# Performance work log

Hardware: AMD Instinct MI355X
Metric: run time of the kernel (lower is better)

Reference implementation:

```python
import jax, jax.numpy as jnp
import numpy as np

EPS = 1e-5
DEPTH = 3
NQ = 12


def _bn(x, g, b):
    # BatchNorm1d in training mode: batch statistics, biased variance
    mu = x.mean(0)
    var = x.var(0)
    return (x - mu) / jnp.sqrt(var + EPS) * g + b


def _ln(x, g, b):
    mu = x.mean(-1, keepdims=True)
    var = x.var(-1, keepdims=True)
    return (x - mu) / jnp.sqrt(var + EPS) * g + b


def _apply_1q(s, U, q):
    # s: [B, 2^NQ] complex; U: [2,2] (shared) or [B,2,2] (per-sample); qubit q = q-th MSB
    B = s.shape[0]
    s = s.reshape(B, 2 ** q, 2, -1)
    sub = 'ij,bajc->baic' if U.ndim == 2 else 'bij,bajc->baic'
    return jnp.einsum(sub, U, s).reshape(B, -1)


def _apply_cry(s, theta, c):
    # controlled-Ry(theta): control qubit c, target qubit c+1 (adjacent)
    B = s.shape[0]
    s = s.reshape(B, 2 ** c, 2, 2, -1)
    co = jnp.cos(theta / 2).astype(s.dtype)
    si = jnp.sin(theta / 2).astype(s.dtype)
    s1 = s[:, :, 1]  # control = |1> block
    new1 = jnp.stack([co * s1[:, :, 0] - si * s1[:, :, 1],
                      si * s1[:, :, 0] + co * s1[:, :, 1]], axis=2)
    s = jnp.concatenate([s[:, :, :1], new1[:, :, None]], axis=2)
    return s.reshape(B, -1)


def _measure(s):
    # P(qubit q measures |1>) for each qubit
    p = jnp.abs(s) ** 2  # [B, 2^NQ]
    B = p.shape[0]
    probs = [p.reshape(B, 2 ** q, 2, -1).sum(axis=(1, 3))[:, 1] for q in range(NQ)]
    return jnp.stack(probs, axis=1)  # [B, NQ]


def _rot_mats(rot):
    # fused Rz(rz) @ Ry(ry) @ Rx(rx) for each (depth, qubit) -> [DEPTH, NQ, 2, 2]
    hx, hy, hz = rot[..., 0] / 2, rot[..., 1] / 2, rot[..., 2] / 2
    cx, sx = jnp.cos(hx), jnp.sin(hx)
    Rx = jnp.stack([jnp.stack([cx + 0j, -1j * sx], -1),
                    jnp.stack([-1j * sx, cx + 0j], -1)], -2)
    cy, sy = jnp.cos(hy), jnp.sin(hy)
    Ry = jnp.stack([jnp.stack([cy, -sy], -1),
                    jnp.stack([sy, cy], -1)], -2).astype(jnp.complex64)
    ez = jnp.exp(-1j * hz)
    z0 = jnp.zeros_like(ez)
    Rz = jnp.stack([jnp.stack([ez, z0], -1),
                    jnp.stack([z0, jnp.conj(ez)], -1)], -2)
    return jnp.einsum('...ij,...jk,...kl->...il', Rz, Ry, Rx).astype(jnp.complex64)


def _quantum_layer(x, We, be, gi, bi, rot, ent, Wd, bd, go, bo):
    e = jnp.tanh(_bn(x @ We.T + be, gi, bi))  # [B, NQ]
    nrm = jnp.linalg.norm(e, axis=1, keepdims=True)
    a = jnp.where(nrm > 0, e / nrm, e)        # per-sample L2-normalized amplitudes
    B = x.shape[0]
    s = jnp.zeros((B, 2 ** NQ), jnp.complex64).at[:, 0].set(1.0)
    # amplitude encoding: Ry(2*arcsin(|a|)) then phase pi (sign) if a<0 -> diag(1,-1)@Ry
    ang = 2.0 * jnp.arcsin(jnp.clip(jnp.abs(a), 0.0, 1.0))
    c, si = jnp.cos(ang / 2), jnp.sin(ang / 2)
    sg = jnp.where(a < 0, -1.0, 1.0)
    for q in range(NQ):
        U = jnp.stack([jnp.stack([c[:, q], -si[:, q]], -1),
                       jnp.stack([sg[:, q] * si[:, q], sg[:, q] * c[:, q]], -1)],
                      -2).astype(jnp.complex64)  # [B,2,2]
        s = _apply_1q(s, U, q)
    # parameterized circuit: per-qubit fused Rz.Ry.Rx, then nearest-neighbor CRy chain
    U = _rot_mats(rot)
    for d in range(DEPTH):
        for q in range(NQ):
            s = _apply_1q(s, U[d, q], q)
        for i in range(NQ - 1):
            s = _apply_cry(s, ent[d, i], i)
    m = _measure(s)
    return _bn(m @ Wd.T + bd, go, bo)


def setup_inputs() -> dict:
    key = jax.random.key(0)
    ks = jax.random.split(key, 16)
    B, IN, H1, H2, H3, OUT = 512, 512, 512, 512, 1024, 256

    def lin(k, o, i):
        k1, k2 = jax.random.split(k)
        lim = 1.0 / np.sqrt(i)
        return (jax.random.uniform(k1, (o, i), jnp.float32, -lim, lim),
                jax.random.uniform(k2, (o,), jnp.float32, -lim, lim))

    qWe0, qbe0 = lin(ks[1], NQ, IN)
    qWd0, qbd0 = lin(ks[2], H1, NQ)
    qWe1, qbe1 = lin(ks[3], NQ, H1)
    qWd1, qbd1 = lin(ks[4], H2, NQ)
    W2, b2 = lin(ks[5], H3, H2)
    Wo, bo = lin(ks[6], OUT, H3)
    return {
        'x': jax.random.normal(ks[0], (B, IN), jnp.float32),
        'qWe0': qWe0, 'qbe0': qbe0,
        'qgi0': jnp.ones(NQ), 'qbi0': jnp.zeros(NQ),
        'rot0': 0.1 * jax.random.normal(ks[7], (DEPTH, NQ, 3), jnp.float32),
        'ent0': 0.1 * jax.random.normal(ks[8], (DEPTH, NQ - 1), jnp.float32),
        'qWd0': qWd0, 'qbd0': qbd0,
        'qgo0': jnp.ones(H1), 'qbo0': jnp.zeros(H1),
        'qWe1': qWe1, 'qbe1': qbe1,
        'qgi1': jnp.ones(NQ), 'qbi1': jnp.zeros(NQ),
        'rot1': 0.1 * jax.random.normal(ks[9], (DEPTH, NQ, 3), jnp.float32),
        'ent1': 0.1 * jax.random.normal(ks[10], (DEPTH, NQ - 1), jnp.float32),
        'qWd1': qWd1, 'qbd1': qbd1,
        'qgo1': jnp.ones(H2), 'qbo1': jnp.zeros(H2),
        'W2': W2, 'b2': b2, 'ln2g': jnp.ones(H3), 'ln2b': jnp.zeros(H3),
        'Wo': Wo, 'bo': bo, 'lnog': jnp.ones(OUT), 'lnob': jnp.zeros(OUT),
    }


def reference(x, qWe0, qbe0, qgi0, qbi0, rot0, ent0, qWd0, qbd0, qgo0, qbo0,
              qWe1, qbe1, qgi1, qbi1, rot1, ent1, qWd1, qbd1, qgo1, qbo1,
              W2, b2, ln2g, ln2b, Wo, bo, lnog, lnob):
    h = _quantum_layer(x, qWe0, qbe0, qgi0, qbi0, rot0, ent0, qWd0, qbd0, qgo0, qbo0)
    h = _quantum_layer(h, qWe1, qbe1, qgi1, qbi1, rot1, ent1, qWd1, qbd1, qgo1, qbo1)
    h = jax.nn.relu(_ln(h @ W2.T + b2, ln2g, ln2b))  # classical block (dropout = identity, eval)
    return _ln(h @ Wo.T + bo, lnog, lnob)
```

## Files before the change

### kernel.cpp

```cpp
#include <hip/hip_runtime.h>
#include <math.h>

#define EPS   1e-5f
#define NQ    12
#define DEPTH 3
#define BATCH 512
#define DIM   4096

__device__ inline float2 cmul(float2 a, float2 b) {
    return make_float2(a.x*b.x - a.y*b.y, a.x*b.y + a.y*b.x);
}
__device__ inline float2 cmac2(float2 ua, float2 s, float2 ub, float2 p) {
    return make_float2(ua.x*s.x - ua.y*s.y + ub.x*p.x - ub.y*p.y,
                       ua.x*s.y + ua.y*s.x + ub.x*p.y + ub.y*p.x);
}
__device__ inline float fast_tanh(float x) {
    float e = __expf(2.f * x);
    return 1.f - 2.f * __builtin_amdgcn_rcpf(e + 1.f);
}

__device__ inline int swz(int a) { return a ^ ((a >> 4) & 15); }

template<int HB> __device__ inline int ampl16(int t, int k) {
    return ((t >> HB) << (HB+4)) | (k << HB) | (t & ((1<<HB)-1));
}

__device__ inline void remap16a(float2* amp, float2* lds,
                                const int* wA, const int* rA) {
    #pragma unroll
    for (int k = 0; k < 16; ++k) lds[wA[k]] = amp[k];
    __syncthreads();
    #pragma unroll
    for (int k = 0; k < 16; ++k) amp[k] = lds[rA[k]];
}

template<int BP>
__device__ inline void one_q(float2* amp, float2 u00, float2 u01, float2 u10, float2 u11) {
    #pragma unroll
    for (int g = 0; g < 8; ++g) {
        const int j0 = ((g >> BP) << (BP+1)) | (g & ((1<<BP)-1));
        const int j1 = j0 | (1 << BP);
        float2 a0 = amp[j0], a1 = amp[j1];
        amp[j0] = cmac2(u00, a0, u01, a1);
        amp[j1] = cmac2(u10, a0, u11, a1);
    }
}

template<int CB, int TB>
__device__ inline void cry_rr(float2* amp, float co, float si) {
    #pragma unroll
    for (int m = 0; m < 16; ++m) {
        if (((m >> CB) & 1) && !((m >> TB) & 1)) {
            const int j1 = m | (1 << TB);
            float2 a0 = amp[m], a1 = amp[j1];
            amp[m]  = make_float2(co*a0.x - si*a1.x, co*a0.y - si*a1.y);
            amp[j1] = make_float2(si*a0.x + co*a1.x, si*a0.y + co*a1.y);
        }
    }
}

template<int TB>
__device__ inline void crysel16(float2* amp, int ctrl, float co, float si) {
    float co2 = ctrl ? co : 1.f;
    float s2  = ctrl ? si : 0.f;
    #pragma unroll
    for (int m = 0; m < 16; ++m) {
        if (!((m >> TB) & 1)) {
            const int j1 = m | (1 << TB);
            float2 a0 = amp[m], a1 = amp[j1];
            amp[m]  = make_float2(co2*a0.x - s2*a1.x, co2*a0.y - s2*a1.y);
            amp[j1] = make_float2(s2*a0.x + co2*a1.x, s2*a0.y + co2*a1.y);
        }
    }
}

__device__ void consts_body(int t,
        const float* rot0, const float* ent0, const float* rot1, const float* ent1,
        float2* Uc, float2* Cc) {
    if (t < 72) {
        int layer = t / 36, rem = t % 36, d = rem / 12, q = rem % 12;
        const float* rot = layer ? rot1 : rot0;
        float hx = 0.5f * rot[(d*NQ + q)*3 + 0];
        float hy = 0.5f * rot[(d*NQ + q)*3 + 1];
        float hz = 0.5f * rot[(d*NQ + q)*3 + 2];
        float cx = cosf(hx), sx = sinf(hx);
        float cy = cosf(hy), sy = sinf(hy);
        float2 m00 = make_float2( cy*cx,  sy*sx);
        float2 m01 = make_float2(-sy*cx, -cy*sx);
        float2 m10 = make_float2( sy*cx, -cy*sx);
        float2 m11 = make_float2( cy*cx, -sy*sx);
        float2 ez  = make_float2(cosf(hz), -sinf(hz));
        float2 ezc = make_float2(ez.x, -ez.y);
        float2* U = Uc + t*4;
        U[0] = cmul(ez,  m00);
        U[1] = cmul(ez,  m01);
        U[2] = cmul(ezc, m10);
        U[3] = cmul(ezc, m11);
    } else if (t < 72 + 66) {
        int idx = t - 72, layer = idx / 33, rem = idx % 33;
        const float* ent = layer ? ent1 : ent0;
        float th = 0.5f * ent[rem];
        Cc[idx] = make_float2(cosf(th), sinf(th));
    }
}

__global__ __launch_bounds__(256) void encode0_consts_kernel(
        const float* __restrict__ X, const float* __restrict__ We,
        const float* __restrict__ be, float* __restrict__ Yraw,
        const float* __restrict__ rot0, const float* __restrict__ ent0,
        const float* __restrict__ rot1, const float* __restrict__ ent1,
        float2* __restrict__ Uc, float2* __restrict__ Cc,
        float* __restrict__ Yraw1z) {
    int tid = threadIdx.x;
    if (blockIdx.x == 128) {
        consts_body(tid, rot0, ent0, rot1, ent1, Uc, Cc);
        for (int i = tid; i < BATCH*NQ; i += 256) Yraw1z[i] = 0.f;
        return;
    }
    __shared__ float w[NQ][512];
    {
        const float4* src = (const float4*)We;
        float4* dst = (float4*)&w[0][0];
        #pragma unroll
        for (int i = tid; i < NQ*128; i += 256) dst[i] = src[i];
    }
    __syncthreads();
    int wave = tid >> 6, lane = tid & 63;
    int b = blockIdx.x * 4 + wave;
    const float4* xr = (const float4*)(X + (size_t)b * 512);
    float acc[NQ] = {};
    #pragma unroll
    for (int j = 0; j < 2; ++j) {
        float4 xv = xr[lane + 64*j];
        #pragma unroll
        for (int q = 0; q < NQ; ++q) {
            float4 wv = ((const float4*)&w[q][0])[lane + 64*j];
            acc[q] += xv.x*wv.x + xv.y*wv.y + xv.z*wv.z + xv.w*wv.w;
        }
    }
    #pragma unroll
    for (int q = 0; q < NQ; ++q) {
        float v = acc[q];
        #pragma unroll
        for (int off = 32; off; off >>= 1) v += __shfl_xor(v, off);
        if (lane == q) Yraw[b*NQ + q] = v + be[q];
    }
}

__global__ __launch_bounds__(256, 2) void qsim3w_kernel(
        const float* __restrict__ Yraw, const float* __restrict__ gi,
        const float* __restrict__ bi, const float2* __restrict__ UcAll,
        const float2* __restrict__ CcAll, int layer,
        float* __restrict__ mout) {
    int blk = blockIdx.x, t = threadIdx.x;
    const float2* Uc = UcAll + layer * DEPTH * NQ * 4;
    const float2* Cc = CcAll + layer * DEPTH * (NQ - 1);
    __shared__ float2 lds2[2][DIM];
    __shared__ float sred[96];

    int A8[16], A4[16], A0[16];
    #pragma unroll
    for (int k = 0; k < 16; ++k) {
        A8[k] = swz(ampl16<8>(t, k));
        A4[k] = swz(ampl16<4>(t, k));
        A0[k] = swz(ampl16<0>(t, k));
    }

    float sum[NQ] = {}, sq[NQ] = {};
    {
        const float4* Y4 = (const float4*)Yraw;
        #pragma unroll
        for (int j = 0; j < 6; ++j) {
            float4 v = Y4[t*6 + j];
            int q0 = (j*4) % 12;
            sum[q0+0]+=v.x; sq[q0+0]+=v.x*v.x;
            sum[q0+1]+=v.y; sq[q0+1]+=v.y*v.y;
            sum[q0+2]+=v.z; sq[q0+2]+=v.z*v.z;
            sum[q0+3]+=v.w; sq[q0+3]+=v.w*v.w;
        }
    }
    int lane = t & 63, wave = t >> 6;
    #pragma unroll
    for (int q = 0; q < NQ; ++q) {
        #pragma unroll
        for (int off = 32; off; off >>= 1) {
            sum[q] += __shfl_xor(sum[q], off);
            sq[q]  += __shfl_xor(sq[q],  off);
        }
    }
    if (lane == 0) {
        #pragma unroll
        for (int q = 0; q < NQ; ++q) {
            sred[wave*24 + q]      = sum[q];
            sred[wave*24 + 12 + q] = sq[q];
        }
    }
    __syncthreads();
    float a[NQ]; float n2 = 0.f;
    const float* yr = Yraw + blk*NQ;
    #pragma unroll
    for (int q = 0; q < NQ; ++q) {
        float s  = sred[q]    + sred[24+q] + sred[48+q] + sred[72+q];
        float s2 = sred[12+q] + sred[36+q] + sred[60+q] + sred[84+q];
        float mu  = s  * (1.f/512.f);
        float var = s2 * (1.f/512.f) - mu*mu;
        float val = (yr[q] - mu) * rsqrtf(var + EPS) * gi[q] + bi[q];
        a[q] = fast_tanh(val);
        n2 += a[q]*a[q];
    }
    float scn = (n2 > 0.f) ? rsqrtf(n2) : 1.f;
    #pragma unroll
    for (int q = 0; q < NQ; ++q) a[q] *= scn;

    float2 v0[NQ], v1[NQ];
    #pragma unroll
    for (int q = 0; q < NQ; ++q) {
        float sv = fminf(fabsf(a[q]), 1.f);
        float c  = sqrtf(fmaxf(1.f - sv*sv, 0.f));
        float ss = (a[q] < 0.f) ? -sv : sv;
        const float2* U = Uc + q*4;
        v0[q] = make_float2(U[0].x*c + U[1].x*ss, U[0].y*c + U[1].y*ss);
        v1[q] = make_float2(U[2].x*c + U[3].x*ss, U[2].y*c + U[3].y*ss);
    }
    float2 common = make_float2(1.f, 0.f);
    #pragma unroll
    for (int j = 0; j < 8; ++j)
        common = cmul(common, ((t >> j) & 1) ? v1[11-j] : v0[11-j]);
    float2 amp[16];
    amp[0] = common;
    #pragma unroll
    for (int mb = 0; mb < 4; ++mb) {
        const int qb = 3 - mb;
        #pragma unroll
        for (int k = 0; k < (1<<mb); ++k) {
            amp[k | (1<<mb)] = cmul(amp[k], v1[qb]);
            amp[k]           = cmul(amp[k], v0[qb]);
        }
    }

    int rb = 0;
    for (int d = 0; d < DEPTH; ++d) {
        const float2* Ud = Uc + d*NQ*4;
        const float2* Cd = Cc + d*(NQ-1);
        if (d > 0) {
            remap16a(amp, lds2[rb], A0, A8); rb ^= 1;
            one_q<3>(amp, Ud[0],  Ud[1],  Ud[2],  Ud[3]);
            one_q<2>(amp, Ud[4],  Ud[5],  Ud[6],  Ud[7]);
            one_q<1>(amp, Ud[8],  Ud[9],  Ud[10], Ud[11]);
            one_q<0>(amp, Ud[12], Ud[13], Ud[14], Ud[15]);
        }
        cry_rr<3,2>(amp, Cd[0].x, Cd[0].y);
        cry_rr<2,1>(amp, Cd[1].x, Cd[1].y);
        cry_rr<1,0>(amp, Cd[2].x, Cd[2].y);
        remap16a(amp, lds2[rb], A8, A4); rb ^= 1;
        if (d > 0) {
            one_q<3>(amp, Ud[16], Ud[17], Ud[18], Ud[19]);
            one_q<2>(amp, Ud[20], Ud[21], Ud[22], Ud[23]);
            one_q<1>(amp, Ud[24], Ud[25], Ud[26], Ud[27]);
            one_q<0>(amp, Ud[28], Ud[29], Ud[30], Ud[31]);
        }
        crysel16<3>(amp, (t >> 4) & 1, Cd[3].x, Cd[3].y);
        cry_rr<3,2>(amp, Cd[4].x, Cd[4].y);
        cry_rr<2,1>(amp, Cd[5].x, Cd[5].y);
        cry_rr<1,0>(amp, Cd[6].x, Cd[6].y);
        remap16a(amp, lds2[rb], A4, A0); rb ^= 1;
        if (d > 0) {
            one_q<3>(amp, Ud[32], Ud[33], Ud[34], Ud[35]);
            one_q<2>(amp, Ud[36], Ud[37], Ud[38], Ud[39]);
            one_q<1>(amp, Ud[40], Ud[41], Ud[42], Ud[43]);
            one_q<0>(amp, Ud[44], Ud[45], Ud[46], Ud[47]);
        }
        crysel16<3>(amp, t & 1, Cd[7].x, Cd[7].y);
        cry_rr<3,2>(amp, Cd[8].x,  Cd[8].y);
        cry_rr<2,1>(amp, Cd[9].x,  Cd[9].y);
        cry_rr<1,0>(amp, Cd[10].x, Cd[10].y);
    }

    float msum = 0.f, p8 = 0.f, p9 = 0.f, p10 = 0.f, p11 = 0.f;
    #pragma unroll
    for (int k = 0; k < 16; ++k) {
        float m = amp[k].x*amp[k].x + amp[k].y*amp[k].y;
        msum += m;
        if (k & 8) p8  += m;
        if (k & 4) p9  += m;
        if (k & 2) p10 += m;
        if (k & 1) p11 += m;
    }
    #pragma unroll
    for (int q = 0; q < NQ; ++q) {
        float v;
        if (q < 8)        v = ((t >> (7-q)) & 1) ? msum : 0.f;
        else if (q == 8)  v = p8;
        else if (q == 9)  v = p9;
        else if (q == 10) v = p10;
        else              v = p11;
        #pragma unroll
        for (int off = 32; off; off >>= 1) v += __shfl_xor(v, off);
        if (lane == 0) sred[q*4 + wave] = v;
    }
    __syncthreads();
    if (t < NQ)
        mout[blk*16 + t] = sred[t*4] + sred[t*4+1] + sred[t*4+2] + sred[t*4+3];
}

__global__ __launch_bounds__(512) void decode_kernel(
        const float* __restrict__ m, const float* __restrict__ Wd,
        const float* __restrict__ bd, const float* __restrict__ go,
        const float* __restrict__ bo, float* __restrict__ outT) {
    int h = blockIdx.x, b = threadIdx.x;
    __shared__ float2 red[8];
    float4 r0 = *(const float4*)(m + (size_t)b*16 + 0);
    float4 r1 = *(const float4*)(m + (size_t)b*16 + 4);
    float4 r2 = *(const float4*)(m + (size_t)b*16 + 8);
    const float4* W4 = (const float4*)(Wd + h*NQ);
    float4 w0 = W4[0], w1 = W4[1], w2 = W4[2];
    float z = bd[h]
        + r0.x*w0.x + r0.y*w0.y + r0.z*w0.z + r0.w*w0.w
        + r1.x*w1.x + r1.y*w1.y + r1.z*w1.z + r1.w*w1.w
        + r2.x*w2.x + r2.y*w2.y + r2.z*w2.z + r2.w*w2.w;
    float2 v = make_float2(z, z*z);
    int lane = b & 63, wave = b >> 6;
    for (int off = 32; off; off >>= 1) { v.x += __shfl_down(v.x, off); v.y += __shfl_down(v.y, off); }
    if (lane == 0) red[wave] = v;
    __syncthreads();
    float s = 0.f, s2 = 0.f;
    #pragma unroll
    for (int wv = 0; wv < 8; ++wv) { s += red[wv].x; s2 += red[wv].y; }
    float mu  = s  * (1.f/512.f);
    float var = s2 * (1.f/512.f) - mu*mu;
    outT[(size_t)h*BATCH + b] = (z - mu) * rsqrtf(var + EPS) * go[h] + bo[h];
}

__global__ __launch_bounds__(256) void encode1_kernel(
        const float* __restrict__ h1T, const float* __restrict__ We,
        const float* __restrict__ be, float* __restrict__ Yraw1) {
    __shared__ float w[NQ][512];
    __shared__ float red[4*64*NQ];
    int tid = threadIdx.x, blk = blockIdx.x;
    {
        const float4* src = (const float4*)We;
        float4* dst = (float4*)&w[0][0];
        #pragma unroll
        for (int i = tid; i < NQ*128; i += 256) dst[i] = src[i];
    }
    __syncthreads();
    int kc = blk >> 3, bc = blk & 7;
    int bl = tid & 63, hg = tid >> 6;
    int b = bc*64 + bl;
    float acc[NQ] = {};
    #pragma unroll
    for (int i = 0; i < 16; ++i) {
        int h = kc*64 + hg*16 + i;
        float xv = h1T[(size_t)h*512 + b];
        #pragma unroll
        for (int q = 0; q < NQ; ++q) acc[q] += xv * w[q][h];
    }
    #pragma unroll
    for (int q = 0; q < NQ; ++q) red[(hg*64 + bl)*NQ + q] = acc[q];
    __syncthreads();
    for (int i = tid; i < 64*NQ; i += 256) {
        int bl2 = i / NQ, q = i - bl2*NQ;
        float v = red[bl2*NQ+q] + red[(64+bl2)*NQ+q] + red[(128+bl2)*NQ+q] + red[(192+bl2)*NQ+q];
        if (kc == 0) v += be[q];
        atomicAdd(&Yraw1[(size_t)(bc*64 + bl2)*NQ + q], v);
    }
}

__global__ __launch_bounds__(256) void gemm1_kernel(
        const float* __restrict__ AT, const float* __restrict__ W,
        float* __restrict__ Cpart) {
    __shared__ float As[2][32][64];
    __shared__ float Bs[2][32][68];
    const int b0 = blockIdx.x * 64, j0 = blockIdx.y * 64;
    const int kbase = blockIdx.z * 128;
    float* C = Cpart + (size_t)blockIdx.z * 512 * 1024;
    const int tid = threadIdx.x;
    const int tr = tid >> 4, tc = tid & 15;
    const int a_kk = tid >> 4, a_f4 = tid & 15;
    const int b_jj = tid >> 3, b_k4 = (tid & 7) * 4;
    float4 ra0, ra1, rb0, rb1;
    float acc[4][4] = {};
    {
        const int k0 = kbase;
        ra0 = *(const float4*)(AT + (size_t)(k0 + a_kk)*512 + b0 + a_f4*4);
        ra1 = *(const float4*)(AT + (size_t)(k0 + a_kk + 16)*512 + b0 + a_f4*4);
        rb0 = *(const float4*)(W + (size_t)(j0 + b_jj)*512 + k0 + b_k4);
        rb1 = *(const float4*)(W + (size_t)(j0 + b_jj + 32)*512 + k0 + b_k4);
        *(float4*)&As[0][a_kk][a_f4*4] = ra0;
        *(float4*)&As[0][a_kk+16][a_f4*4] = ra1;
        Bs[0][b_k4+0][b_jj] = rb0.x; Bs[0][b_k4+1][b_jj] = rb0.y;
        Bs[0][b_k4+2][b_jj] = rb0.z; Bs[0][b_k4+3][b_jj] = rb0.w;
        Bs[0][b_k4+0][b_jj+32] = rb1.x; Bs[0][b_k4+1][b_jj+32] = rb1.y;
        Bs[0][b_k4+2][b_jj+32] = rb1.z; Bs[0][b_k4+3][b_jj+32] = rb1.w;
    }
    __syncthreads();
    for (int s = 0; s < 4; ++s) {
        if (s < 3) {
            const int k0 = kbase + (s+1)*32;
            ra0 = *(const float4*)(AT + (size_t)(k0 + a_kk)*512 + b0 + a_f4*4);
            ra1 = *(const float4*)(AT + (size_t)(k0 + a_kk + 16)*512 + b0 + a_f4*4);
            rb0 = *(const float4*)(W + (size_t)(j0 + b_jj)*512 + k0 + b_k4);
            rb1 = *(const float4*)(W + (size_t)(j0 + b_jj + 32)*512 + k0 + b_k4);
        }
        const int bf = s & 1;
        #pragma unroll
        for (int kk = 0; kk < 32; ++kk) {
            float4 a  = *(const float4*)&As[bf][kk][tr*4];
            float4 bv = *(const float4*)&Bs[bf][kk][tc*4];
            acc[0][0] += a.x*bv.x; acc[0][1] += a.x*bv.y; acc[0][2] += a.x*bv.z; acc[0][3] += a.x*bv.w;
            acc[1][0] += a.y*bv.x; acc[1][1] += a.y*bv.y; acc[1][2] += a.y*bv.z; acc[1][3] += a.y*bv.w;
            acc[2][0] += a.z*bv.x; acc[2][1] += a.z*bv.y; acc[2][2] += a.z*bv.z; acc[2][3] += a.z*bv.w;
            acc[3][0] += a.w*bv.x; acc[3][1] += a.w*bv.y; acc[3][2] += a.w*bv.z; acc[3][3] += a.w*bv.w;
        }
        if (s < 3) {
            const int nb = bf ^ 1;
            *(float4*)&As[nb][a_kk][a_f4*4] = ra0;
            *(float4*)&As[nb][a_kk+16][a_f4*4] = ra1;
            Bs[nb][b_k4+0][b_jj] = rb0.x; Bs[nb][b_k4+1][b_jj] = rb0.y;
            Bs[nb][b_k4+2][b_jj] = rb0.z; Bs[nb][b_k4+3][b_jj] = rb0.w;
            Bs[nb][b_k4+0][b_jj+32] = rb1.x; Bs[nb][b_k4+1][b_jj+32] = rb1.y;
            Bs[nb][b_k4+2][b_jj+32] = rb1.z; Bs[nb][b_k4+3][b_jj+32] = rb1.w;
        }
        __syncthreads();
    }
    #pragma unroll
    for (int r = 0; r < 4; ++r) {
        float4 o = make_float4(acc[r][0], acc[r][1], acc[r][2], acc[r][3]);
        *(float4*)(C + (size_t)(b0 + tr*4 + r)*1024 + j0 + tc*4) = o;
    }
}

__global__ __launch_bounds__(256) void ln_relu_kernel(
        const float* __restrict__ P, const float* __restrict__ bias,
        const float* __restrict__ g, const float* __restrict__ be,
        float* __restrict__ Y) {
    int b = blockIdx.x, tid = threadIdx.x;
    __shared__ float2 red[4];
    float v[4];
    #pragma unroll
    for (int j = 0; j < 4; ++j) {
        int col = tid + j*256;
        float t = bias[col];
        #pragma unroll
        for (int z = 0; z < 4; ++z) t += P[(size_t)z*524288 + (size_t)b*1024 + col];
        v[j] = t;
    }
    float2 r = make_float2(v[0]+v[1]+v[2]+v[3],
                           v[0]*v[0]+v[1]*v[1]+v[2]*v[2]+v[3]*v[3]);
    int lane = tid & 63, wave = tid >> 6;
    for (int off = 32; off; off >>= 1) { r.x += __shfl_down(r.x, off); r.y += __shfl_down(r.y, off); }
    if (lane == 0) red[wave] = r;
    __syncthreads();
    float s = red[0].x + red[1].x + red[2].x + red[3].x;
    float s2 = red[0].y + red[1].y + red[2].y + red[3].y;
    float mu  = s  * (1.f/1024.f);
    float var = s2 * (1.f/1024.f) - mu*mu;
    float inv = rsqrtf(var + EPS);
    float* yr = Y + (size_t)b * 1024;
    #pragma unroll
    for (int j = 0; j < 4; ++j) {
        int col = tid + j*256;
        yr[col] = fmaxf((v[j]-mu)*inv*g[col] + be[col], 0.f);
    }
}

__global__ __launch_bounds__(256) void gemm2_kernel(
        const float* __restrict__ Amat, const float* __restrict__ W,
        float* __restrict__ Cpart) {
    __shared__ __align__(16) char smem[27000];
    float (*As)[32][36] = (float(*)[32][36])smem;
    float (*Bs)[32][68] = (float(*)[32][68])(smem + 9216);
    const int b0 = blockIdx.x * 32, j0 = blockIdx.y * 64;
    const int kbase = blockIdx.z * 128;
    float* C = Cpart + (size_t)blockIdx.z * 512 * 256;
    const int tid = threadIdx.x;
    const int tr = tid >> 4, tc = tid & 15;
    const int l_r = tid >> 3, l_k4 = (tid & 7) * 4;
    float4 ra0, rb0, rb1;
    float acc[2][4] = {};
    {
        const int k0 = kbase;
        ra0 = *(const float4*)(Amat + (size_t)(b0 + l_r)*1024 + k0 + l_k4);
        rb0 = *(const float4*)(W + (size_t)(j0 + l_r)*1024 + k0 + l_k4);
        rb1 = *(const float4*)(W + (size_t)(j0 + l_r + 32)*1024 + k0 + l_k4);
        As[0][l_k4+0][l_r] = ra0.x; As[0][l_k4+1][l_r] = ra0.y;
        As[0][l_k4+2][l_r] = ra0.z; As[0][l_k4+3][l_r] = ra0.w;
        Bs[0][l_k4+0][l_r] = rb0.x; Bs[0][l_k4+1][l_r] = rb0.y;
        Bs[0][l_k4+2][l_r] = rb0.z; Bs[0][l_k4+3][l_r] = rb0.w;
        Bs[0][l_k4+0][l_r+32] = rb1.x; Bs[0][l_k4+1][l_r+32] = rb1.y;
        Bs[0][l_k4+2][l_r+32] = rb1.z; Bs[0][l_k4+3][l_r+32] = rb1.w;
    }
    __syncthreads();
    for (int s = 0; s < 4; ++s) {
        if (s < 3) {
            const int k0 = kbase + (s+1)*32;
            ra0 = *(const float4*)(Amat + (size_t)(b0 + l_r)*1024 + k0 + l_k4);
            rb0 = *(const float4*)(W + (size_t)(j0 + l_r)*1024 + k0 + l_k4);
            rb1 = *(const float4*)(W + (size_t)(j0 + l_r + 32)*1024 + k0 + l_k4);
        }
        const int bf = s & 1;
        #pragma unroll
        for (int kk = 0; kk < 32; ++kk) {
            float a0 = As[bf][kk][tr*2], a1 = As[bf][kk][tr*2+1];
            float4 bv = *(const float4*)&Bs[bf][kk][tc*4];
            acc[0][0] += a0*bv.x; acc[0][1] += a0*bv.y; acc[0][2] += a0*bv.z; acc[0][3] += a0*bv.w;
            acc[1][0] += a1*bv.x; acc[1][1] += a1*bv.y; acc[1][2] += a1*bv.z; acc[1][3] += a1*bv.w;
        }
        if (s < 3) {
            const int nb = bf ^ 1;
            As[nb][l_k4+0][l_r] = ra0.x; As[nb][l_k4+1][l_r] = ra0.y;
            As[nb][l_k4+2][l_r] = ra0.z; As[nb][l_k4+3][l_r] = ra0.w;
            Bs[nb][l_k4+0][l_r] = rb0.x; Bs[nb][l_k4+1][l_r] = rb0.y;
            Bs[nb][l_k4+2][l_r] = rb0.z; Bs[nb][l_k4+3][l_r] = rb0.w;
            Bs[nb][l_k4+0][l_r+32] = rb1.x; Bs[nb][l_k4+1][l_r+32] = rb1.y;
            Bs[nb][l_k4+2][l_r+32] = rb1.z; Bs[nb][l_k4+3][l_r+32] = rb1.w;
        }
        __syncthreads();
    }
    #pragma unroll
    for (int r = 0; r < 2; ++r) {
        float4 o = make_float4(acc[r][0], acc[r][1], acc[r][2], acc[r][3]);
        *(float4*)(C + (size_t)(b0 + tr*2 + r)*256 + j0 + tc*4) = o;
    }
}

__global__ __launch_bounds__(256) void ln_out_kernel(
        const float* __restrict__ P, const float* __restrict__ bias,
        const float* __restrict__ g, const float* __restrict__ be,
        float* __restrict__ Y) {
    int b = blockIdx.x, tid = threadIdx.x;
    __shared__ float2 red[4];
    float v0 = bias[tid];
    #pragma unroll
    for (int z = 0; z < 8; ++z) v0 += P[(size_t)z*131072 + (size_t)b*256 + tid];
    float2 v = make_float2(v0, v0*v0);
    int lane = tid & 63, wave = tid >> 6;
    for (int off = 32; off; off >>= 1) { v.x += __shfl_down(v.x, off); v.y += __shfl_down(v.y, off); }
    if (lane == 0) red[wave] = v;
    __syncthreads();
    float s = red[0].x + red[1].x + red[2].x + red[3].x;
    float s2 = red[0].y + red[1].y + red[2].y + red[3].y;
    float mu  = s  * (1.f/256.f);
    float var = s2 * (1.f/256.f) - mu*mu;
    Y[(size_t)b*256 + tid] = (v0 - mu) * rsqrtf(var + EPS) * g[tid] + be[tid];
}

extern "C" void kernel_launch(void* const* d_in, const int* in_sizes, int n_in,
                              void* d_out, int out_size, void* d_ws, size_t ws_size,
                              hipStream_t stream) {
    const float* x    = (const float*)d_in[0];
    const float* qWe0 = (const float*)d_in[1];
    const float* qbe0 = (const float*)d_in[2];
    const float* qgi0 = (const float*)d_in[3];
    const float* qbi0 = (const float*)d_in[4];
    const float* rot0 = (const float*)d_in[5];
    const float* ent0 = (const float*)d_in[6];
    const float* qWd0 = (const float*)d_in[7];
    const float* qbd0 = (const float*)d_in[8];
    const float* qgo0 = (const float*)d_in[9];
    const float* qbo0 = (const float*)d_in[10];
    const float* qWe1 = (const float*)d_in[11];
    const float* qbe1 = (const float*)d_in[12];
    const float* qgi1 = (const float*)d_in[13];
    const float* qbi1 = (const float*)d_in[14];
    const float* rot1 = (const float*)d_in[15];
    const float* ent1 = (const float*)d_in[16];
    const float* qWd1 = (const float*)d_in[17];
    const float* qbd1 = (const float*)d_in[18];
    const float* qgo1 = (const float*)d_in[19];
    const float* qbo1 = (const float*)d_in[20];
    const float* W2   = (const float*)d_in[21];
    const float* b2   = (const float*)d_in[22];
    const float* ln2g = (const float*)d_in[23];
    const float* ln2b = (const float*)d_in[24];
    const float* Wo   = (const float*)d_in[25];
    const float* bo   = (const float*)d_in[26];
    const float* lnog = (const float*)d_in[27];
    const float* lnob = (const float*)d_in[28];
    float* out = (float*)d_out;
    float* ws  = (float*)d_ws;

    float2* Uc   = (float2*)ws;
    float2* Cc   = Uc + 288;
    float* Yraw0 = ws + 1024;
    float* m0    = ws + 8192;
    float* Yraw1 = ws + 16384;
    float* m1    = ws + 24576;
    float* h1T   = ws + 65536;
    float* h2T   = ws + 589824;
    float* t3p   = ws + 851968;
    float* t3n   = ws + 2949120;
    float* t4p   = ws + 3473408;

    hipLaunchKernelGGL(encode0_consts_kernel, dim3(129), dim3(256), 0, stream,
                       x, qWe0, qbe0, Yraw0, rot0, ent0, rot1, ent1, Uc, Cc, Yraw1);
    hipLaunchKernelGGL(qsim3w_kernel, dim3(512), dim3(256), 0, stream,
                       Yraw0, qgi0, qbi0, Uc, Cc, 0, m0);
    hipLaunchKernelGGL(decode_kernel, dim3(512), dim3(512), 0, stream,
                       m0, qWd0, qbd0, qgo0, qbo0, h1T);
    hipLaunchKernelGGL(encode1_kernel, dim3(64), dim3(256), 0, stream,
                       h1T, qWe1, qbe1, Yraw1);
    hipLaunchKernelGGL(qsim3w_kernel, dim3(512), dim3(256), 0, stream,
                       Yraw1, qgi1, qbi1, Uc, Cc, 1, m1);
    hipLaunchKernelGGL(decode_kernel, dim3(512), dim3(512), 0, stream,
                       m1, qWd1, qbd1, qgo1, qbo1, h2T);
    hipLaunchKernelGGL(gemm1_kernel, dim3(8, 16, 4), dim3(256), 0, stream,
                       h2T, W2, t3p);
    hipLaunchKernelGGL(ln_relu_kernel, dim3(512), dim3(256), 0, stream,
                       t3p, b2, ln2g, ln2b, t3n);
    hipLaunchKernelGGL(gemm2_kernel, dim3(16, 4, 8), dim3(256), 0, stream,
                       t3n, Wo, t4p);
    hipLaunchKernelGGL(ln_out_kernel, dim3(512), dim3(256), 0, stream,
                       t4p, bo, lnog, lnob, out);
}
```

Measured before the change: 220.2 us.

## Fuse decode0 and encode1 algebraically into a single-block mid kernel

Replaces the layer-0 decode (512x512 BatchNorm output) and the layer-1 encode GEMM with one single-block kernel. It uses the fact that decode is affine in the 12-dim measurement vector, so batch stats follow from the mean and covariance of m0, and the encode can be folded into a 12x12 matrix plus a bias. The second qsim then reads precomputed normalised angles instead of recomputing BatchNorm and tanh, and the Yraw1 zeroing and atomics go away. In exchange, all of this runs on one workgroup with serial loops, and the covariance-based variance may change floating-point rounding.

New measurement: 229.4 us. +4.2%, slower.

```diff
diff --git a/kernel.cpp b/kernel.cpp
--- a/kernel.cpp
+++ b/kernel.cpp
@@ -109,12 +109,10 @@
         const float* __restrict__ be, float* __restrict__ Yraw,
         const float* __restrict__ rot0, const float* __restrict__ ent0,
         const float* __restrict__ rot1, const float* __restrict__ ent1,
-        float2* __restrict__ Uc, float2* __restrict__ Cc,
-        float* __restrict__ Yraw1z) {
+        float2* __restrict__ Uc, float2* __restrict__ Cc) {
     int tid = threadIdx.x;
     if (blockIdx.x == 128) {
         consts_body(tid, rot0, ent0, rot1, ent1, Uc, Cc);
-        for (int i = tid; i < BATCH*NQ; i += 256) Yraw1z[i] = 0.f;
         return;
     }
     __shared__ float w[NQ][512];
@@ -147,8 +145,9 @@
     }
 }
 
+template<int MODE>
 __global__ __launch_bounds__(256, 2) void qsim3w_kernel(
-        const float* __restrict__ Yraw, const float* __restrict__ gi,
+        const float* __restrict__ Yin, const float* __restrict__ gi,
         const float* __restrict__ bi, const float2* __restrict__ UcAll,
         const float2* __restrict__ CcAll, int layer,
         float* __restrict__ mout) {
@@ -166,51 +165,59 @@
         A0[k] = swz(ampl16<0>(t, k));
     }
 
-    float sum[NQ] = {}, sq[NQ] = {};
-    {
-        const float4* Y4 = (const float4*)Yraw;
-        #pragma unroll
-        for (int j = 0; j < 6; ++j) {
-            float4 v = Y4[t*6 + j];
-            int q0 = (j*4) % 12;
-            sum[q0+0]+=v.x; sq[q0+0]+=v.x*v.x;
-            sum[q0+1]+=v.y; sq[q0+1]+=v.y*v.y;
-            sum[q0+2]+=v.z; sq[q0+2]+=v.z*v.z;
-            sum[q0+3]+=v.w; sq[q0+3]+=v.w*v.w;
-        }
-    }
-    int lane = t & 63, wave = t >> 6;
-    #pragma unroll
-    for (int q = 0; q < NQ; ++q) {
-        #pragma unroll
-        for (int off = 32; off; off >>= 1) {
-            sum[q] += __shfl_xor(sum[q], off);
-            sq[q]  += __shfl_xor(sq[q],  off);
-        }
-    }
-    if (lane == 0) {
+    float a[NQ];
+    if (MODE == 0) {
+        float sum[NQ] = {}, sq[NQ] = {};
+        {
+            const float4* Y4 = (const float4*)Yin;
+            #pragma unroll
+            for (int j = 0; j < 6; ++j) {
+                float4 v = Y4[t*6 + j];
+                int q0 = (j*4) % 12;
+                sum[q0+0]+=v.x; sq[q0+0]+=v.x*v.x;
+                sum[q0+1]+=v.y; sq[q0+1]+=v.y*v.y;
+                sum[q0+2]+=v.z; sq[q0+2]+=v.z*v.z;
+                sum[q0+3]+=v.w; sq[q0+3]+=v.w*v.w;
+            }
+        }
+        int lane = t & 63, wave = t >> 6;
         #pragma unroll
         for (int q = 0; q < NQ; ++q) {
-            sred[wave*24 + q]      = sum[q];
-            sred[wave*24 + 12 + q] = sq[q];
-        }
-    }
-    __syncthreads();
-    float a[NQ]; float n2 = 0.f;
-    const float* yr = Yraw + blk*NQ;
-    #pragma unroll
-    for (int q = 0; q < NQ; ++q) {
-        float s  = sred[q]    + sred[24+q] + sred[48+q] + sred[72+q];
-        float s2 = sred[12+q] + sred[36+q] + sred[60+q] + sred[84+q];
-        float mu  = s  * (1.f/512.f);
-        float var = s2 * (1.f/512.f) - mu*mu;
-        float val = (yr[q] - mu) * rsqrtf(var + EPS) * gi[q] + bi[q];
-        a[q] = fast_tanh(val);
-        n2 += a[q]*a[q];
-    }
-    float scn = (n2 > 0.f) ? rsqrtf(n2) : 1.f;
-    #pragma unroll
-    for (int q = 0; q < NQ; ++q) a[q] *= scn;
+            #pragma unroll
+            for (int off = 32; off; off >>= 1) {
+                sum[q] += __shfl_xor(sum[q], off);
+                sq[q]  += __shfl_xor(sq[q],  off);
+            }
+        }
+        if (lane == 0) {
+            #pragma unroll
+            for (int q = 0; q < NQ; ++q) {
+                sred[wave*24 + q]      = sum[q];
+                sred[wave*24 + 12 + q] = sq[q];
+            }
+        }
+        __syncthreads();
+        float n2 = 0.f;
+        const float* yr = Yin + blk*NQ;
+        #pragma unroll
+        for (int q = 0; q < NQ; ++q) {
+            float s  = sred[q]    + sred[24+q] + sred[48+q] + sred[72+q];
+            float s2 = sred[12+q] + sred[36+q] + sred[60+q] + sred[84+q];
+            float mu  = s  * (1.f/512.f);
+            float var = s2 * (1.f/512.f) - mu*mu;
+            float val = (yr[q] - mu) * rsqrtf(var + EPS) * gi[q] + bi[q];
+            a[q] = fast_tanh(val);
+            n2 += a[q]*a[q];
+        }
+        float scn = (n2 > 0.f) ? rsqrtf(n2) : 1.f;
+        #pragma unroll
+        for (int q = 0; q < NQ; ++q) a[q] *= scn;
+        __syncthreads();
+    } else {
+        const float* ar = Yin + blk*16;
+        #pragma unroll
+        for (int q = 0; q < NQ; ++q) a[q] = ar[q];
+    }
 
     float2 v0[NQ], v1[NQ];
     #pragma unroll
@@ -286,6 +293,7 @@
         if (k & 2) p10 += m;
         if (k & 1) p11 += m;
     }
+    int lane = t & 63, wave = t >> 6;
     #pragma unroll
     for (int q = 0; q < NQ; ++q) {
         float v;
@@ -301,6 +309,127 @@
     __syncthreads();
     if (t < NQ)
         mout[blk*16 + t] = sred[t*4] + sred[t*4+1] + sred[t*4+2] + sred[t*4+3];
+}
+
+__global__ __launch_bounds__(512) void fuse_mid_kernel(
+        const float* __restrict__ m0,
+        const float* __restrict__ Wd, const float* __restrict__ bd,
+        const float* __restrict__ go, const float* __restrict__ bo,
+        const float* __restrict__ We1, const float* __restrict__ be1,
+        const float* __restrict__ gi1, const float* __restrict__ bi1,
+        float* __restrict__ A1) {
+    const int t = threadIdx.x;
+    __shared__ float mc[512][12];
+    __shared__ float su[512];
+    __shared__ float part[312][4];
+    __shared__ float mbar_s[12], C_s[144], E_s[144], F_s[12], mY[12], vY[12];
+
+    float mr[12];
+    {
+        float4 r0 = *(const float4*)(m0 + (size_t)t*16 + 0);
+        float4 r1 = *(const float4*)(m0 + (size_t)t*16 + 4);
+        float4 r2 = *(const float4*)(m0 + (size_t)t*16 + 8);
+        mr[0]=r0.x; mr[1]=r0.y; mr[2]=r0.z; mr[3]=r0.w;
+        mr[4]=r1.x; mr[5]=r1.y; mr[6]=r1.z; mr[7]=r1.w;
+        mr[8]=r2.x; mr[9]=r2.y; mr[10]=r2.z; mr[11]=r2.w;
+        #pragma unroll
+        for (int j = 0; j < 12; ++j) mc[t][j] = mr[j];
+    }
+    __syncthreads();
+    if (t < 48) {
+        int j = t >> 2, c = t & 3;
+        float s = 0.f;
+        for (int b = c*128; b < c*128 + 128; ++b) s += mc[b][j];
+        part[j][c] = s;
+    }
+    __syncthreads();
+    if (t < 12) mbar_s[t] = (part[t][0]+part[t][1]+part[t][2]+part[t][3]) * (1.f/512.f);
+    __syncthreads();
+    if (t < 312) {
+        int p = t >> 2, c = t & 3;
+        int j = 0, rem = p;
+        while (rem >= 12 - j) { rem -= 12 - j; ++j; }
+        int k = j + rem;
+        float s = 0.f;
+        for (int b = c*128; b < c*128 + 128; ++b) s += mc[b][j]*mc[b][k];
+        part[p][c] = s;
+    }
+    __syncthreads();
+    if (t < 78) {
+        int p = t, j = 0, rem = p;
+        while (rem >= 12 - j) { rem -= 12 - j; ++j; }
+        int k = j + rem;
+        float cv = (part[p][0]+part[p][1]+part[p][2]+part[p][3]) * (1.f/512.f)
+                   - mbar_s[j]*mbar_s[k];
+        C_s[j*12+k] = cv; C_s[k*12+j] = cv;
+    }
+    __syncthreads();
+    {
+        float wd[12];
+        #pragma unroll
+        for (int j = 0; j < 12; ++j) wd[j] = Wd[t*12 + j];
+        float mu = bd[t];
+        #pragma unroll
+        for (int j = 0; j < 12; ++j) mu += wd[j]*mbar_s[j];
+        float var = 0.f;
+        #pragma unroll
+        for (int j = 0; j < 12; ++j) {
+            float cj = 0.f;
+            #pragma unroll
+            for (int k = 0; k < 12; ++k) cj += C_s[j*12+k]*wd[k];
+            var += wd[j]*cj;
+        }
+        float s = go[t] * rsqrtf(var + EPS);
+        su[t] = bo[t] + s*(bd[t] - mu);
+        #pragma unroll
+        for (int j = 0; j < 12; ++j) mc[t][j] = s*wd[j];
+    }
+    __syncthreads();
+    if (t < 144) {
+        int q = t / 12, j = t - (t/12)*12;
+        const float* we = We1 + q*512;
+        float s = 0.f;
+        for (int h = 0; h < 512; ++h) s += we[h]*mc[h][j];
+        E_s[t] = s;
+    } else if (t < 156) {
+        int q = t - 144;
+        const float* we = We1 + q*512;
+        float s = be1[q];
+        for (int h = 0; h < 512; ++h) s += we[h]*su[h];
+        F_s[q] = s;
+    }
+    __syncthreads();
+    if (t < 12) {
+        float me = F_s[t];
+        #pragma unroll
+        for (int j = 0; j < 12; ++j) me += E_s[t*12+j]*mbar_s[j];
+        mY[t] = me;
+        float var = 0.f;
+        #pragma unroll
+        for (int j = 0; j < 12; ++j) {
+            float cj = 0.f;
+            #pragma unroll
+            for (int k = 0; k < 12; ++k) cj += C_s[j*12+k]*E_s[t*12+k];
+            var += E_s[t*12+j]*cj;
+        }
+        vY[t] = var;
+    }
+    __syncthreads();
+    {
+        float a[12]; float n2 = 0.f;
+        #pragma unroll
+        for (int q = 0; q < 12; ++q) {
+            float y = F_s[q];
+            #pragma unroll
+            for (int j = 0; j < 12; ++j) y += mr[j]*E_s[q*12+j];
+            float val = (y - mY[q]) * rsqrtf(vY[q] + EPS) * gi1[q] + bi1[q];
+            a[q] = fast_tanh(val);
+            n2 += a[q]*a[q];
+        }
+        float scn = (n2 > 0.f) ? rsqrtf(n2) : 1.f;
+        #pragma unroll
+        for (int q = 0; q < 12; ++q) A1[(size_t)t*16 + q] = a[q]*scn;
+    }
 }
 
 __global__ __launch_bounds__(512) void decode_kernel(
@@ -329,41 +458,6 @@
     float mu  = s  * (1.f/512.f);
     float var = s2 * (1.f/512.f) - mu*mu;
     outT[(size_t)h*BATCH + b] = (z - mu) * rsqrtf(var + EPS) * go[h] + bo[h];
-}
-
-__global__ __launch_bounds__(256) void encode1_kernel(
-        const float* __restrict__ h1T, const float* __restrict__ We,
-        const float* __restrict__ be, float* __restrict__ Yraw1) {
-    __shared__ float w[NQ][512];
-    __shared__ float red[4*64*NQ];
-    int tid = threadIdx.x, blk = blockIdx.x;
-    {
-        const float4* src = (const float4*)We;
-        float4* dst = (float4*)&w[0][0];
-        #pragma unroll
-        for (int i = tid; i < NQ*128; i += 256) dst[i] = src[i];
-    }
-    __syncthreads();
-    int kc = blk >> 3, bc = blk & 7;
-    int bl = tid & 63, hg = tid >> 6;
-    int b = bc*64 + bl;
-    float acc[NQ] = {};
-    #pragma unroll
-    for (int i = 0; i < 16; ++i) {
-        int h = kc*64 + hg*16 + i;
-        float xv = h1T[(size_t)h*512 + b];
-        #pragma unroll
-        for (int q = 0; q < NQ; ++q) acc[q] += xv * w[q][h];
-    }
-    #pragma unroll
-    for (int q = 0; q < NQ; ++q) red[(hg*64 + bl)*NQ + q] = acc[q];
-    __syncthreads();
-    for (int i = tid; i < 64*NQ; i += 256) {
-        int bl2 = i / NQ, q = i - bl2*NQ;
-        float v = red[bl2*NQ+q] + red[(64+bl2)*NQ+q] + red[(128+bl2)*NQ+q] + red[(192+bl2)*NQ+q];
-        if (kc == 0) v += be[q];
-        atomicAdd(&Yraw1[(size_t)(bc*64 + bl2)*NQ + q], v);
-    }
 }
 
 __global__ __launch_bounds__(256) void gemm1_kernel(
@@ -584,24 +678,21 @@
     float2* Cc   = Uc + 288;
     float* Yraw0 = ws + 1024;
     float* m0    = ws + 8192;
-    float* Yraw1 = ws + 16384;
+    float* A1    = ws + 16384;
     float* m1    = ws + 24576;
-    float* h1T   = ws + 65536;
     float* h2T   = ws + 589824;
     float* t3p   = ws + 851968;
     float* t3n   = ws + 2949120;
     float* t4p   = ws + 3473408;
 
     hipLaunchKernelGGL(encode0_consts_kernel, dim3(129), dim3(256), 0, stream,
-                       x, qWe0, qbe0, Yraw0, rot0, ent0, rot1, ent1, Uc, Cc, Yraw1);
-    hipLaunchKernelGGL(qsim3w_kernel, dim3(512), dim3(256), 0, stream,
+                       x, qWe0, qbe0, Yraw0, rot0, ent0, rot1, ent1, Uc, Cc);
+    hipLaunchKernelGGL(qsim3w_kernel<0>, dim3(512), dim3(256), 0, stream,
                        Yraw0, qgi0, qbi0, Uc, Cc, 0, m0);
-    hipLaunchKernelGGL(decode_kernel, dim3(512), dim3(512), 0, stream,
-                       m0, qWd0, qbd0, qgo0, qbo0, h1T);
-    hipLaunchKernelGGL(encode1_kernel, dim3(64), dim3(256), 0, stream,
-                       h1T, qWe1, qbe1, Yraw1);
-    hipLaunchKernelGGL(qsim3w_kernel, dim3(512), dim3(256), 0, stream,
-                       Yraw1, qgi1, qbi1, Uc, Cc, 1, m1);
+    hipLaunchKernelGGL(fuse_mid_kernel, dim3(1), dim3(512), 0, stream,
+                       m0, qWd0, qbd0, qgo0, qbo0, qWe1, qbe1, qgi1, qbi1, A1);
+    hipLaunchKernelGGL(qsim3w_kernel<1>, dim3(512), dim3(256), 0, stream,
+                       A1, qgi1, qbi1, Uc, Cc, 1, m1);
     hipLaunchKernelGGL(decode_kernel, dim3(512), dim3(512), 0, stream,
                        m1, qWd1, qbd1, qgo1, qbo1, h2T);
     hipLaunchKernelGGL(gemm1_kernel, dim3(8, 16, 4), dim3(256), 0, stream,
```
